# Kernel tuning notes

Hardware: AMD Instinct MI355X
Metric: run time of the kernel (lower is better)

The kernel has to match this reference:

```python
import jax, jax.numpy as jnp
import numpy as np

N = 8192
F_IN = 128
D = 128
NEG_SLOPE = 0.2  # cfg.negativeslope (standard GAT value)
MASK_FILL = -9e15


def setup_inputs() -> dict:
    key = jax.random.key(0)
    k1, k2, k3, k4 = jax.random.split(key, 4)
    A = jax.random.randint(k1, (N, N), 0, 2, dtype=jnp.int32)
    X = jax.random.normal(k2, (N, F_IN), dtype=jnp.float32)
    # glorot init for Ws, xavier_uniform(gain=1.414) for a
    lim_w = float(np.sqrt(6.0 / (F_IN + D)))
    Ws = jax.random.uniform(k3, (F_IN, D), minval=-lim_w, maxval=lim_w, dtype=jnp.float32)
    lim_a = 1.414 * float(np.sqrt(6.0 / (2 * D + 1)))
    a = jax.random.uniform(k4, (2 * D, 1), minval=-lim_a, maxval=lim_a, dtype=jnp.float32)
    return {"A": A, "X": X, "Ws": Ws, "a": a}


def reference(A, X, Ws, a):
    # Wh: [N, D]
    Wh = X @ Ws
    d = Wh.shape[-1]
    # additive attention: e_ij = leaky_relu(Wh_i . a1 + Wh_j . a2)
    e1 = Wh @ a[:d]          # [N, 1]
    e2 = Wh @ a[d:]          # [N, 1]
    e = jax.nn.leaky_relu(e1 + e2.T, negative_slope=NEG_SLOPE)  # [N, N]
    e = jnp.where(A > 0, e, MASK_FILL)
    attn = jax.nn.softmax(e, axis=1)  # row-wise over neighbors
    H = attn @ Wh            # [N, D]
    return H
```

## Files before the change

### kernel.cpp

```cpp
#include <hip/hip_runtime.h>
#include <hip/hip_bf16.h>

#define NN 8192
#define DD 128

typedef __attribute__((ext_vector_type(8))) short short8;
typedef __attribute__((ext_vector_type(4))) float f32x4;
typedef unsigned int u32;

__device__ __forceinline__ ushort f2bf(float f) {
    __hip_bfloat16 h = __float2bfloat16(f);
    return *(ushort*)&h;
}

__device__ __forceinline__ void async_ld16(const void* g, void* l) {
    __builtin_amdgcn_global_load_lds(
        (const __attribute__((address_space(1))) u32*)g,
        (__attribute__((address_space(3))) u32*)l, 16, 0, 0);
}

__global__ __launch_bounds__(256) void k1_gemm(const float* __restrict__ X,
                                               const float* __restrict__ Ws,
                                               float* __restrict__ Wh) {
    __shared__ float lWs[128 * 132];
    __shared__ float lX[32 * 132];
    int t = threadIdx.x, bx = blockIdx.x;
    const float4* Ws4 = (const float4*)Ws;
    const float4* X4 = (const float4*)X;
    for (int j = 0; j < 16; ++j) {
        int u = j * 256 + t;
        int k = u >> 5, c4 = u & 31;
        *(float4*)&lWs[k * 132 + c4 * 4] = Ws4[u];
    }
    for (int j = 0; j < 4; ++j) {
        int u = j * 256 + t;
        int r = u >> 5, c4 = u & 31;
        *(float4*)&lX[r * 132 + c4 * 4] = X4[bx * 1024 + u];
    }
    __syncthreads();
    int r0 = (t >> 5) * 4, c0 = (t & 31) * 4;
    float acc[4][4];
#pragma unroll
    for (int i = 0; i < 4; ++i)
#pragma unroll
        for (int j = 0; j < 4; ++j) acc[i][j] = 0.f;
#pragma unroll 4
    for (int k = 0; k < 128; ++k) {
        float4 wv = *(const float4*)&lWs[k * 132 + c0];
        float x0 = lX[(r0 + 0) * 132 + k];
        float x1 = lX[(r0 + 1) * 132 + k];
        float x2 = lX[(r0 + 2) * 132 + k];
        float x3 = lX[(r0 + 3) * 132 + k];
#pragma unroll
        for (int j = 0; j < 4; ++j) {
            acc[0][j] += x0 * ((const float*)&wv)[j];
            acc[1][j] += x1 * ((const float*)&wv)[j];
            acc[2][j] += x2 * ((const float*)&wv)[j];
            acc[3][j] += x3 * ((const float*)&wv)[j];
        }
    }
#pragma unroll
    for (int i = 0; i < 4; ++i)
        *(float4*)&Wh[(size_t)(bx * 32 + r0 + i) * 128 + c0] =
            (float4){acc[i][0], acc[i][1], acc[i][2], acc[i][3]};
}

__global__ __launch_bounds__(256) void k2_prep(const float* __restrict__ Wh,
                                               const float* __restrict__ a,
                                               ushort* __restrict__ WhT,
                                               float* __restrict__ C1,
                                               float* __restrict__ C1s,
                                               float2* __restrict__ E2) {
    __shared__ float lT[128 * 65];
    __shared__ float la[256];
    int t = threadIdx.x;
    int i0 = blockIdx.x * 64;
    la[t] = a[t];
    for (int j = 0; j < 32; ++j) {
        int u = j * 256 + t;
        int r = u >> 7, c = u & 127;
        lT[c * 65 + r] = Wh[(size_t)(i0 + r) * 128 + c];
    }
    __syncthreads();
    int r = t >> 2, q = t & 3;
    float s1 = 0.f, s2 = 0.f;
    for (int j = 0; j < 32; ++j) {
        int d = q * 32 + j;
        float v = lT[d * 65 + r];
        s1 += v * la[d];
        s2 += v * la[128 + d];
    }
    s1 += __shfl_xor(s1, 1); s1 += __shfl_xor(s1, 2);
    s2 += __shfl_xor(s2, 1); s2 += __shfl_xor(s2, 2);
    if (q == 0) {
        int i = i0 + r;
        C1[i]  = __expf(s1);
        C1s[i] = __expf(0.2f * s1);
        E2[i]  = make_float2(__expf(s2), __expf(0.2f * s2));
    }
    int d = t >> 1, hf = t & 1;
    __attribute__((aligned(16))) ushort tmp[32];
#pragma unroll
    for (int s = 0; s < 32; ++s) tmp[s] = f2bf(lT[d * 65 + hf * 32 + s]);
    uint4* dst = (uint4*)&WhT[(size_t)d * NN + i0 + hf * 32];
    const uint4* srcv = (const uint4*)tmp;
#pragma unroll
    for (int s = 0; s < 4; ++s) dst[s] = srcv[s];
}

__global__ __launch_bounds__(256) void k0_pack(const int* __restrict__ A,
                                               u32* __restrict__ Ap,
                                               float* __restrict__ Hp,
                                               float* __restrict__ Lp) {
    u32 u = blockIdx.x * 256 + threadIdx.x;
    if (u < (u32)(NN * DD)) Hp[u] = 0.f;
    if (u < (u32)NN) Lp[u] = 0.f;
    u32 kt = u >> 15;
    u32 row = (u >> 2) & (NN - 1);
    u32 kg = u & 3;
    const int* base = A + (size_t)row * NN + kt * 128 + kg * 8;
    u32 d = 0;
#pragma unroll
    for (int tp = 0; tp < 4; ++tp) {
        int4 lo = *(const int4*)(base + tp * 32);
        int4 hi = *(const int4*)(base + tp * 32 + 4);
        u32 b = 0;
        b |= (lo.x != 0) ? 1u : 0u;
        b |= (lo.y != 0) ? 2u : 0u;
        b |= (lo.z != 0) ? 4u : 0u;
        b |= (lo.w != 0) ? 8u : 0u;
        b |= (hi.x != 0) ? 16u : 0u;
        b |= (hi.y != 0) ? 32u : 0u;
        b |= (hi.z != 0) ? 64u : 0u;
        b |= (hi.w != 0) ? 128u : 0u;
        d |= b << (8 * tp);
    }
    Ap[u] = d;
}

__global__ __launch_bounds__(512, 4) void k3_main(
    const u32* __restrict__ Ap, const ushort* __restrict__ WhT,
    const float* __restrict__ C1, const float* __restrict__ C1s,
    const float2* __restrict__ E2,
    float* __restrict__ Hp, float* __restrict__ Lp) {

    __shared__ __align__(16) char lB[2 * 32768];
    __shared__ __align__(16) char lE[2 * 1024];

    int tid = threadIdx.x;
    int lane = tid & 63;
    int w = tid >> 6;
    int n = lane & 15;
    int kg = lane >> 4;

    int bx = blockIdx.x;
    int kb = blockIdx.y;
    int rb = bx * 128 + w * 16;
    int row = rb + n;
    int kt0 = kb * 8;

    float c1 = C1[row], c1s = C1s[row];

    const char* srcB[4];
    char* dstB[4];
#pragma unroll
    for (int i = 0; i < 4; ++i) {
        int p = 4 * w + i;
        int c = p & 7, tp = p >> 3;
        srcB[i] = (const char*)(WhT + (size_t)(c * 16 + n) * NN +
                                (size_t)kt0 * 128 + tp * 32 + kg * 8);
        dstB[i] = lB + p * 1024 + lane * 16;
    }
    const char* srcE = (const char*)(E2 + (size_t)kt0 * 128) + lane * 16;

    const u32* pA = Ap + ((size_t)kt0 * NN + row) * 4 + kg;
    u32 a_cur = pA[0];
    u32 a_nxt = 0;

#pragma unroll
    for (int i = 0; i < 4; ++i) async_ld16(srcB[i], dstB[i]);
    if (w == 0) async_ld16(srcE, lE + lane * 16);

    short8 ones;
#pragma unroll
    for (int j = 0; j < 8; ++j) ones[j] = (short)0x3F80;

    f32x4 acc[8];
#pragma unroll
    for (int c = 0; c < 8; ++c) acc[c] = (f32x4){0.f, 0.f, 0.f, 0.f};
    f32x4 accl = (f32x4){0.f, 0.f, 0.f, 0.f};

    __syncthreads();

    for (int kt = 0; kt < 8; ++kt) {
        int buf = kt & 1;
        if (kt < 7) {
            int bo = (buf ^ 1) * 32768;
#pragma unroll
            for (int i = 0; i < 4; ++i)
                async_ld16(srcB[i] + (kt + 1) * 256, dstB[i] + bo);
            if (w == 0)
                async_ld16(srcE + (kt + 1) * 1024, lE + (buf ^ 1) * 1024 + lane * 16);
            a_nxt = pA[(size_t)(kt + 1) * (NN * 4)];
        }
        const char* bB = lB + buf * 32768;
        const float* bE = (const float*)(lE + buf * 1024);
#pragma unroll
        for (int tp = 0; tp < 4; ++tp) {
            const float4* ev = (const float4*)(bE + (tp * 32 + kg * 8) * 2);
            float pe[16];
            *(float4*)(pe + 0)  = ev[0];
            *(float4*)(pe + 4)  = ev[1];
            *(float4*)(pe + 8)  = ev[2];
            *(float4*)(pe + 12) = ev[3];
            u32 ab = (a_cur >> (tp * 8)) & 0xffu;
            short8 af;
#pragma unroll
            for (int u = 0; u < 8; ++u) {
                float wv = fmaxf(c1 * pe[2 * u], c1s * pe[2 * u + 1]);
                af[u] = ((ab >> u) & 1u) ? (short)f2bf(wv) : (short)0;
            }
            const short8* bb = (const short8*)(bB + tp * 8192);
#pragma unroll
            for (int c = 0; c < 8; ++c)
                acc[c] = __builtin_amdgcn_mfma_f32_16x16x32_bf16(
                    af, bb[c * 64 + lane], acc[c], 0, 0, 0);
            accl = __builtin_amdgcn_mfma_f32_16x16x32_bf16(af, ones, accl, 0, 0, 0);
        }
        a_cur = a_nxt;
        __syncthreads();
    }

#pragma unroll
    for (int c = 0; c < 8; ++c)
#pragma unroll
        for (int r = 0; r < 4; ++r)
            atomicAdd(&Hp[(size_t)(rb + kg * 4 + r) * DD + c * 16 + n], acc[c][r]);
    if (n == 0)
#pragma unroll
        for (int r = 0; r < 4; ++r)
            atomicAdd(&Lp[rb + kg * 4 + r], accl[r]);
}

__global__ void k4_final(const float* __restrict__ Hp, const float* __restrict__ Lp,
                         float* __restrict__ out) {
    int idx = blockIdx.x * 256 + threadIdx.x;
    out[idx] = Hp[idx] / Lp[idx >> 7];
}

extern "C" void kernel_launch(void* const* d_in, const int* in_sizes, int n_in,
                              void* d_out, int out_size, void* d_ws, size_t ws_size,
                              hipStream_t stream) {
    const int*   A  = (const int*)d_in[0];
    const float* X  = (const float*)d_in[1];
    const float* Ws = (const float*)d_in[2];
    const float* a  = (const float*)d_in[3];
    float* out = (float*)d_out;

    char* ws = (char*)d_ws;
    u32*    Ap  = (u32*)(ws);
    float*  Wh  = (float*)(ws);
    ushort* WhT = (ushort*)(ws + (8u << 20));
    float*  C1  = (float*)(ws + (10u << 20));
    float*  C1s = (float*)(ws + (10u << 20) + (32u << 10));
    float2* E2  = (float2*)(ws + (10u << 20) + (64u << 10));
    float*  Hp  = (float*)(ws + (10u << 20) + (128u << 10));
    float*  Lp  = (float*)(ws + (14u << 20) + (128u << 10));

    k1_gemm<<<256, 256, 0, stream>>>(X, Ws, Wh);
    k2_prep<<<128, 256, 0, stream>>>(Wh, a, WhT, C1, C1s, E2);
    k0_pack<<<8192, 256, 0, stream>>>(A, Ap, Hp, Lp);
    k3_main<<<dim3(64, 8), 512, 0, stream>>>(Ap, WhT, C1, C1s, E2, Hp, Lp);
    k4_final<<<4096, 256, 0, stream>>>(Hp, Lp, out);
}
```

Baseline: 451.2 us.

## Give each wave two row tiles and replace atomics with per-split partial sums

k3_main now runs 256 threads per block, and each wave computes 32 rows instead of 16, so every B fragment read from LDS feeds two MFMAs and each wave loads twice as many WhT tiles. The atomicAdd split-K reduction is replaced by plain stores into 8 per-kb partial buffers, which k4_final sums before dividing. This also removes the zeroing of Hp/Lp from k0_pack. The cost is more accumulator registers, fewer waves per CU, and about 32MB of extra partial-buffer traffic in the final kernel.

Result: no change. 446.3 us (-1.1%).

```diff
diff --git a/kernel.cpp b/kernel.cpp
--- a/kernel.cpp
+++ b/kernel.cpp
@@ -109,12 +109,8 @@
 }
 
 __global__ __launch_bounds__(256) void k0_pack(const int* __restrict__ A,
-                                               u32* __restrict__ Ap,
-                                               float* __restrict__ Hp,
-                                               float* __restrict__ Lp) {
+                                               u32* __restrict__ Ap) {
     u32 u = blockIdx.x * 256 + threadIdx.x;
-    if (u < (u32)(NN * DD)) Hp[u] = 0.f;
-    if (u < (u32)NN) Lp[u] = 0.f;
     u32 kt = u >> 15;
     u32 row = (u >> 2) & (NN - 1);
     u32 kg = u & 3;
@@ -138,7 +134,7 @@
     Ap[u] = d;
 }
 
-__global__ __launch_bounds__(512, 4) void k3_main(
+__global__ __launch_bounds__(256, 2) void k3_main(
     const u32* __restrict__ Ap, const ushort* __restrict__ WhT,
     const float* __restrict__ C1, const float* __restrict__ C1s,
     const float2* __restrict__ E2,
@@ -155,40 +151,43 @@
 
     int bx = blockIdx.x;
     int kb = blockIdx.y;
-    int rb = bx * 128 + w * 16;
-    int row = rb + n;
+    int rb = bx * 128 + w * 32;
     int kt0 = kb * 8;
 
-    float c1 = C1[row], c1s = C1s[row];
-
-    const char* srcB[4];
-    char* dstB[4];
-#pragma unroll
-    for (int i = 0; i < 4; ++i) {
-        int p = 4 * w + i;
-        int c = p & 7, tp = p >> 3;
-        srcB[i] = (const char*)(WhT + (size_t)(c * 16 + n) * NN +
-                                (size_t)kt0 * 128 + tp * 32 + kg * 8);
-        dstB[i] = lB + p * 1024 + lane * 16;
+    float c1_0 = C1[rb + n],      c1s_0 = C1s[rb + n];
+    float c1_1 = C1[rb + 16 + n], c1s_1 = C1s[rb + 16 + n];
+
+    const char* srcB[8];
+    char* dstB[8];
+#pragma unroll
+    for (int i = 0; i < 8; ++i) {
+        srcB[i] = (const char*)(WhT + (size_t)(i * 16 + n) * NN +
+                                (size_t)kt0 * 128 + w * 32 + kg * 8);
+        dstB[i] = lB + (w * 8 + i) * 1024 + lane * 16;
     }
     const char* srcE = (const char*)(E2 + (size_t)kt0 * 128) + lane * 16;
 
-    const u32* pA = Ap + ((size_t)kt0 * NN + row) * 4 + kg;
-    u32 a_cur = pA[0];
-    u32 a_nxt = 0;
-
-#pragma unroll
-    for (int i = 0; i < 4; ++i) async_ld16(srcB[i], dstB[i]);
+    const u32* pA0 = Ap + ((size_t)kt0 * NN + rb + n) * 4 + kg;
+    const u32* pA1 = pA0 + 64;
+    u32 a_cur0 = pA0[0], a_cur1 = pA1[0];
+    u32 a_nxt0 = 0, a_nxt1 = 0;
+
+#pragma unroll
+    for (int i = 0; i < 8; ++i) async_ld16(srcB[i], dstB[i]);
     if (w == 0) async_ld16(srcE, lE + lane * 16);
 
     short8 ones;
 #pragma unroll
     for (int j = 0; j < 8; ++j) ones[j] = (short)0x3F80;
 
-    f32x4 acc[8];
-#pragma unroll
-    for (int c = 0; c < 8; ++c) acc[c] = (f32x4){0.f, 0.f, 0.f, 0.f};
-    f32x4 accl = (f32x4){0.f, 0.f, 0.f, 0.f};
+    f32x4 acc0[8], acc1[8];
+#pragma unroll
+    for (int c = 0; c < 8; ++c) {
+        acc0[c] = (f32x4){0.f, 0.f, 0.f, 0.f};
+        acc1[c] = (f32x4){0.f, 0.f, 0.f, 0.f};
+    }
+    f32x4 accl0 = (f32x4){0.f, 0.f, 0.f, 0.f};
+    f32x4 accl1 = (f32x4){0.f, 0.f, 0.f, 0.f};
 
     __syncthreads();
 
@@ -197,11 +196,12 @@
         if (kt < 7) {
             int bo = (buf ^ 1) * 32768;
 #pragma unroll
-            for (int i = 0; i < 4; ++i)
+            for (int i = 0; i < 8; ++i)
                 async_ld16(srcB[i] + (kt + 1) * 256, dstB[i] + bo);
             if (w == 0)
                 async_ld16(srcE + (kt + 1) * 1024, lE + (buf ^ 1) * 1024 + lane * 16);
-            a_nxt = pA[(size_t)(kt + 1) * (NN * 4)];
+            a_nxt0 = pA0[(size_t)(kt + 1) * (NN * 4)];
+            a_nxt1 = pA1[(size_t)(kt + 1) * (NN * 4)];
         }
         const char* bB = lB + buf * 32768;
         const float* bE = (const float*)(lE + buf * 1024);
@@ -213,39 +213,60 @@
             *(float4*)(pe + 4)  = ev[1];
             *(float4*)(pe + 8)  = ev[2];
             *(float4*)(pe + 12) = ev[3];
-            u32 ab = (a_cur >> (tp * 8)) & 0xffu;
-            short8 af;
+            u32 ab0 = (a_cur0 >> (tp * 8)) & 0xffu;
+            u32 ab1 = (a_cur1 >> (tp * 8)) & 0xffu;
+            short8 af0, af1;
 #pragma unroll
             for (int u = 0; u < 8; ++u) {
-                float wv = fmaxf(c1 * pe[2 * u], c1s * pe[2 * u + 1]);
-                af[u] = ((ab >> u) & 1u) ? (short)f2bf(wv) : (short)0;
+                float w0 = fmaxf(c1_0 * pe[2 * u], c1s_0 * pe[2 * u + 1]);
+                float w1 = fmaxf(c1_1 * pe[2 * u], c1s_1 * pe[2 * u + 1]);
+                af0[u] = ((ab0 >> u) & 1u) ? (short)f2bf(w0) : (short)0;
+                af1[u] = ((ab1 >> u) & 1u) ? (short)f2bf(w1) : (short)0;
             }
             const short8* bb = (const short8*)(bB + tp * 8192);
 #pragma unroll
-            for (int c = 0; c < 8; ++c)
-                acc[c] = __builtin_amdgcn_mfma_f32_16x16x32_bf16(
-                    af, bb[c * 64 + lane], acc[c], 0, 0, 0);
-            accl = __builtin_amdgcn_mfma_f32_16x16x32_bf16(af, ones, accl, 0, 0, 0);
-        }
-        a_cur = a_nxt;
+            for (int c = 0; c < 8; ++c) {
+                short8 bf = bb[c * 64 + lane];
+                acc0[c] = __builtin_amdgcn_mfma_f32_16x16x32_bf16(af0, bf, acc0[c], 0, 0, 0);
+                acc1[c] = __builtin_amdgcn_mfma_f32_16x16x32_bf16(af1, bf, acc1[c], 0, 0, 0);
+            }
+            accl0 = __builtin_amdgcn_mfma_f32_16x16x32_bf16(af0, ones, accl0, 0, 0, 0);
+            accl1 = __builtin_amdgcn_mfma_f32_16x16x32_bf16(af1, ones, accl1, 0, 0, 0);
+        }
+        a_cur0 = a_nxt0;
+        a_cur1 = a_nxt1;
         __syncthreads();
     }
 
+    float* Hpb = Hp + (size_t)kb * (NN * DD);
 #pragma unroll
     for (int c = 0; c < 8; ++c)
 #pragma unroll
-        for (int r = 0; r < 4; ++r)
-            atomicAdd(&Hp[(size_t)(rb + kg * 4 + r) * DD + c * 16 + n], acc[c][r]);
-    if (n == 0)
-#pragma unroll
-        for (int r = 0; r < 4; ++r)
-            atomicAdd(&Lp[rb + kg * 4 + r], accl[r]);
+        for (int r = 0; r < 4; ++r) {
+            Hpb[(size_t)(rb + kg * 4 + r) * DD + c * 16 + n]      = acc0[c][r];
+            Hpb[(size_t)(rb + 16 + kg * 4 + r) * DD + c * 16 + n] = acc1[c][r];
+        }
+    if (n == 0) {
+        float* Lpb = Lp + (size_t)kb * NN;
+#pragma unroll
+        for (int r = 0; r < 4; ++r) {
+            Lpb[rb + kg * 4 + r]      = accl0[r];
+            Lpb[rb + 16 + kg * 4 + r] = accl1[r];
+        }
+    }
 }
 
 __global__ void k4_final(const float* __restrict__ Hp, const float* __restrict__ Lp,
                          float* __restrict__ out) {
     int idx = blockIdx.x * 256 + threadIdx.x;
-    out[idx] = Hp[idx] / Lp[idx >> 7];
+    int i = idx >> 7;
+    float sv = 0.f, l = 0.f;
+#pragma unroll
+    for (int kb = 0; kb < 8; ++kb) {
+        sv += Hp[(size_t)kb * (NN * DD) + idx];
+        l  += Lp[(size_t)kb * NN + i];
+    }
+    out[idx] = sv / l;
 }
 
 extern "C" void kernel_launch(void* const* d_in, const int* in_sizes, int n_in,
@@ -265,11 +286,11 @@
     float*  C1s = (float*)(ws + (10u << 20) + (32u << 10));
     float2* E2  = (float2*)(ws + (10u << 20) + (64u << 10));
     float*  Hp  = (float*)(ws + (10u << 20) + (128u << 10));
-    float*  Lp  = (float*)(ws + (14u << 20) + (128u << 10));
+    float*  Lp  = (float*)(ws + (42u << 20) + (128u << 10));
 
     k1_gemm<<<256, 256, 0, stream>>>(X, Ws, Wh);
     k2_prep<<<128, 256, 0, stream>>>(Wh, a, WhT, C1, C1s, E2);
-    k0_pack<<<8192, 256, 0, stream>>>(A, Ap, Hp, Lp);
-    k3_main<<<dim3(64, 8), 512, 0, stream>>>(Ap, WhT, C1, C1s, E2, Hp, Lp);
+    k0_pack<<<8192, 256, 0, stream>>>(A, Ap);
+    k3_main<<<dim3(64, 8), 256, 0, stream>>>(Ap, WhT, C1, C1s, E2, Hp, Lp);
     k4_final<<<4096, 256, 0, stream>>>(Hp, Lp, out);
 }
```
